# Optimization experiments

Hardware: AMD Instinct MI355X
Metric: run time of the kernel (lower is better)

The kernel has to match this reference:

```python
import jax, jax.numpy as jnp
import numpy as np

B, C, H, W = 32, 256, 96, 96
K = 3
PAD = K // 2


def setup_inputs() -> dict:
    key = jax.random.key(0)
    k1, k2, k3 = jax.random.split(key, 3)
    x = jax.random.normal(k1, (B, C, H, W), dtype=jnp.float32)
    # 1x1 conv params collapsed to dense matrices (act on pooled (B,C) vectors)
    w1 = jax.random.normal(k2, (C, C), dtype=jnp.float32) * 0.02
    b1 = jnp.zeros((C,), dtype=jnp.float32)
    w2 = jax.random.normal(k3, (C * K * K, C), dtype=jnp.float32) * 0.02
    b2 = jnp.zeros((C * K * K,), dtype=jnp.float32)
    return {"x": x, "w1": w1, "b1": b1, "w2": w2, "b2": b2}


def reference(x, w1, b1, w2, b2):
    Bs, Cs, Hs, Ws = x.shape
    # dynamic_net: global avg pool -> 1x1 conv -> GELU (exact) -> 1x1 conv
    pooled = x.mean(axis=(2, 3))                       # (B, C)
    h = jax.nn.gelu(pooled @ w1.T + b1, approximate=False)
    wdyn = (h @ w2.T + b2).reshape(Bs, Cs, K * K)      # (B, C, k^2)

    # reflect pad, then fused per-sample/per-channel 3x3 weighted sum
    xp = jnp.pad(x, ((0, 0), (0, 0), (PAD, PAD), (PAD, PAD)), mode="reflect")
    out = jnp.zeros_like(x)
    for i in range(K):
        for j in range(K):
            idx = i * K + j  # matches F.unfold row-major kernel ordering
            out = out + xp[:, :, i:i + Hs, j:j + Ws] * wdyn[:, :, idx, None, None]
    return out
```

## Files before the change

kernel.cpp:

```cpp
#include <hip/hip_runtime.h>
#include <math.h>

#define Bq 32
#define Cq 256
#define Hq 96
#define Wq 96
#define HWq (Hq * Wq)
#define KKq 9
#define CKq (Cq * KKq)
#define NPLANES (Bq * Cq)

typedef float f4 __attribute__((ext_vector_type(4)));

__global__ __launch_bounds__(256) void pool_kernel(const float* __restrict__ x,
                                                   float* __restrict__ pooled) {
    int plane = blockIdx.x;
    const float4* px = (const float4*)(x + (size_t)plane * HWq);
    int t = threadIdx.x;
    float s = 0.f;
#pragma unroll
    for (int i = 0; i < 9; ++i) {
        float4 v = px[t + i * 256];
        s += v.x + v.y + v.z + v.w;
    }
    for (int off = 32; off > 0; off >>= 1) s += __shfl_down(s, off, 64);
    __shared__ float wsum[4];
    if ((t & 63) == 0) wsum[t >> 6] = s;
    __syncthreads();
    if (t == 0) {
        pooled[plane] = (wsum[0] + wsum[1] + wsum[2] + wsum[3]) * (1.0f / HWq);
    }
}

__global__ __launch_bounds__(256) void fc_fused(const float* __restrict__ pooled,
                                                const float* __restrict__ w1,
                                                const float* __restrict__ b1,
                                                const float* __restrict__ w2,
                                                const float* __restrict__ b2,
                                                float* __restrict__ wdyn) {
    int b = blockIdx.y;
    int j = threadIdx.x;
    __shared__ float p[Cq];
    __shared__ float hs[Cq];
    p[j] = pooled[b * Cq + j];
    __syncthreads();
    const float4* wrow = (const float4*)(w1 + (size_t)j * Cq);
    float acc = b1[j];
#pragma unroll 4
    for (int k = 0; k < Cq / 4; ++k) {
        float4 w = wrow[k];
        acc += p[4 * k] * w.x + p[4 * k + 1] * w.y + p[4 * k + 2] * w.z + p[4 * k + 3] * w.w;
    }
    hs[j] = 0.5f * acc * (1.0f + erff(acc * 0.70710678118654752440f));
    __syncthreads();
    int m = blockIdx.x * 256 + j;
    const float4* w2row = (const float4*)(w2 + (size_t)m * Cq);
    float a2 = b2[m];
#pragma unroll 4
    for (int k = 0; k < Cq / 4; ++k) {
        float4 w = w2row[k];
        a2 += hs[4 * k] * w.x + hs[4 * k + 1] * w.y + hs[4 * k + 2] * w.z + hs[4 * k + 3] * w.w;
    }
    wdyn[b * CKq + m] = a2;
}

__global__ __launch_bounds__(256) void conv_kernel(const float* __restrict__ x,
                                                   const float* __restrict__ wdyn,
                                                   float* __restrict__ out) {
    int plane = (NPLANES - 1) - blockIdx.x;
    const float* xp = x + (size_t)plane * HWq;
    float* op = out + (size_t)plane * HWq;
    const float* wd = wdyn + (size_t)plane * KKq;
    float w0 = wd[0], w1 = wd[1], w2 = wd[2];
    float w3 = wd[3], w4 = wd[4], w5 = wd[5];
    float w6 = wd[6], w7 = wd[7], w8 = wd[8];
    int t = threadIdx.x;
#pragma unroll
    for (int it = 0; it < 9; ++it) {
        int g = t + it * 256;
        int hh = g / 24;
        int wq = (g % 24) * 4;
        int rm = (hh == 0) ? 1 : hh - 1;
        int rp = (hh == 95) ? 94 : hh + 1;
        const float* r0 = xp + rm * Wq;
        const float* r1 = xp + hh * Wq;
        const float* r2 = xp + rp * Wq;
        int li = (wq == 0) ? 1 : wq - 1;
        int ri = (wq == 92) ? 94 : wq + 4;
        float4 c0 = *(const float4*)(r0 + wq);
        float4 c1 = *(const float4*)(r1 + wq);
        float4 c2 = *(const float4*)(r2 + wq);
        float l0 = r0[li], l1 = r1[li], l2 = r2[li];
        float q0 = r0[ri], q1 = r1[ri], q2 = r2[ri];
        float4 o;
        o.x = w0 * l0    + w1 * c0.x + w2 * c0.y;
        o.y = w0 * c0.x  + w1 * c0.y + w2 * c0.z;
        o.z = w0 * c0.y  + w1 * c0.z + w2 * c0.w;
        o.w = w0 * c0.z  + w1 * c0.w + w2 * q0;
        o.x += w3 * l1   + w4 * c1.x + w5 * c1.y;
        o.y += w3 * c1.x + w4 * c1.y + w5 * c1.z;
        o.z += w3 * c1.y + w4 * c1.z + w5 * c1.w;
        o.w += w3 * c1.z + w4 * c1.w + w5 * q1;
        o.x += w6 * l2   + w7 * c2.x + w8 * c2.y;
        o.y += w6 * c2.x + w7 * c2.y + w8 * c2.z;
        o.z += w6 * c2.y + w7 * c2.z + w8 * c2.w;
        o.w += w6 * c2.z + w7 * c2.w + w8 * q2;
        __builtin_nontemporal_store(*(f4*)&o, (f4*)(op + (size_t)g * 4));
    }
}

extern "C" void kernel_launch(void* const* d_in, const int* in_sizes, int n_in,
                              void* d_out, int out_size, void* d_ws, size_t ws_size,
                              hipStream_t stream) {
    const float* x  = (const float*)d_in[0];
    const float* w1 = (const float*)d_in[1];
    const float* b1 = (const float*)d_in[2];
    const float* w2 = (const float*)d_in[3];
    const float* b2 = (const float*)d_in[4];
    float* out = (float*)d_out;

    float* pooled = (float*)d_ws;
    float* wdyn   = pooled + Bq * Cq;

    pool_kernel<<<NPLANES, 256, 0, stream>>>(x, pooled);
    fc_fused<<<dim3(CKq / 256, Bq), 256, 0, stream>>>(pooled, w1, b1, w2, b2, wdyn);
    conv_kernel<<<NPLANES, 256, 0, stream>>>(x, wdyn, out);
}
```

Before: 615.1 us.

## Chunk batch into groups for L2 reuse and stage conv planes in LDS

Splits the batch into four chunks of eight samples and runs pool, FC and conv per chunk, so each chunk's slice of x (about 75 MB) may still be cached between pooling and convolution. The conv kernel also copies each 96x96 plane into shared memory before computing the 3x3 stencil, replacing repeated global gathers with LDS reads. The cost is four times as many launches with serialization between chunks, plus a 36 KB shared buffer per block that limits occupancy.

```diff
diff --git a/kernel.cpp b/kernel.cpp
--- a/kernel.cpp
+++ b/kernel.cpp
@@ -9,12 +9,14 @@
 #define KKq 9
 #define CKq (Cq * KKq)
 #define NPLANES (Bq * Cq)
+#define CHB 8
 
 typedef float f4 __attribute__((ext_vector_type(4)));
 
 __global__ __launch_bounds__(256) void pool_kernel(const float* __restrict__ x,
-                                                   float* __restrict__ pooled) {
-    int plane = blockIdx.x;
+                                                   float* __restrict__ pooled,
+                                                   int plane0) {
+    int plane = plane0 + blockIdx.x;
     const float4* px = (const float4*)(x + (size_t)plane * HWq);
     int t = threadIdx.x;
     float s = 0.f;
@@ -37,8 +39,9 @@
                                                 const float* __restrict__ b1,
                                                 const float* __restrict__ w2,
                                                 const float* __restrict__ b2,
-                                                float* __restrict__ wdyn) {
-    int b = blockIdx.y;
+                                                float* __restrict__ wdyn,
+                                                int b0) {
+    int b = b0 + blockIdx.y;
     int j = threadIdx.x;
     __shared__ float p[Cq];
     __shared__ float hs[Cq];
@@ -66,15 +69,26 @@
 
 __global__ __launch_bounds__(256) void conv_kernel(const float* __restrict__ x,
                                                    const float* __restrict__ wdyn,
-                                                   float* __restrict__ out) {
-    int plane = (NPLANES - 1) - blockIdx.x;
+                                                   float* __restrict__ out,
+                                                   int plane0) {
+    int plane = plane0 + blockIdx.x;
     const float* xp = x + (size_t)plane * HWq;
     float* op = out + (size_t)plane * HWq;
     const float* wd = wdyn + (size_t)plane * KKq;
+
+    __shared__ float sx[HWq];
+    int t = threadIdx.x;
+    const float4* px = (const float4*)xp;
+    float4* ps = (float4*)sx;
+#pragma unroll
+    for (int i = 0; i < 9; ++i) {
+        ps[t + i * 256] = px[t + i * 256];
+    }
     float w0 = wd[0], w1 = wd[1], w2 = wd[2];
     float w3 = wd[3], w4 = wd[4], w5 = wd[5];
     float w6 = wd[6], w7 = wd[7], w8 = wd[8];
-    int t = threadIdx.x;
+    __syncthreads();
+
 #pragma unroll
     for (int it = 0; it < 9; ++it) {
         int g = t + it * 256;
@@ -82,9 +96,9 @@
         int wq = (g % 24) * 4;
         int rm = (hh == 0) ? 1 : hh - 1;
         int rp = (hh == 95) ? 94 : hh + 1;
-        const float* r0 = xp + rm * Wq;
-        const float* r1 = xp + hh * Wq;
-        const float* r2 = xp + rp * Wq;
+        const float* r0 = sx + rm * Wq;
+        const float* r1 = sx + hh * Wq;
+        const float* r2 = sx + rp * Wq;
         int li = (wq == 0) ? 1 : wq - 1;
         int ri = (wq == 92) ? 94 : wq + 4;
         float4 c0 = *(const float4*)(r0 + wq);
@@ -122,7 +136,10 @@
     float* pooled = (float*)d_ws;
     float* wdyn   = pooled + Bq * Cq;
 
-    pool_kernel<<<NPLANES, 256, 0, stream>>>(x, pooled);
-    fc_fused<<<dim3(CKq / 256, Bq), 256, 0, stream>>>(pooled, w1, b1, w2, b2, wdyn);
-    conv_kernel<<<NPLANES, 256, 0, stream>>>(x, wdyn, out);
+    for (int ck = 0; ck < Bq / CHB; ++ck) {
+        int p0 = ck * CHB * Cq;
+        pool_kernel<<<CHB * Cq, 256, 0, stream>>>(x, pooled, p0);
+        fc_fused<<<dim3(CKq / 256, CHB), 256, 0, stream>>>(pooled, w1, b1, w2, b2, wdyn, ck * CHB);
+        conv_kernel<<<CHB * Cq, 256, 0, stream>>>(x, wdyn, out, p0);
+    }
 }
```

New measurement: 610.0 us. About the same (-0.8%).
